# Kernel optimization log

Measured on AMD Instinct MI355X. Metric: run time of the kernel, lower is better.

The kernel has to match this reference:

```python
import jax, jax.numpy as jnp
import numpy as np
import math

D_MODEL = 2048
D_STATE = 16
EXPAND = 2
D_INNER = D_MODEL * EXPAND          # 4096
DT_RANK = math.ceil(D_MODEL / 16)   # 128
BATCH, SEQ_LEN = 2, 512


def setup_inputs() -> dict:
    key = jax.random.key(0)
    ks = jax.random.split(key, 6)
    x = jax.random.normal(ks[0], (BATCH, SEQ_LEN, D_INNER), dtype=jnp.float32)
    # A_log such that A = -exp(A_log) is a stable negative-real decay
    A_log = jnp.log(jax.random.uniform(ks[1], (D_INNER, D_STATE), minval=0.5, maxval=16.0, dtype=jnp.float32))
    D = jnp.ones((D_INNER,), dtype=jnp.float32)
    x_proj_w = 0.02 * jax.random.normal(ks[2], (DT_RANK + 2 * D_STATE, D_INNER), dtype=jnp.float32)
    dt_init_std = DT_RANK ** -0.5
    dt_proj_w = jax.random.uniform(ks[3], (D_INNER, DT_RANK), minval=-dt_init_std, maxval=dt_init_std, dtype=jnp.float32)
    # inverse-softplus init of dt bias, dt ~ loguniform[1e-3, 0.1]
    dt = jnp.exp(jax.random.uniform(ks[4], (D_INNER,), dtype=jnp.float32) * (math.log(0.1) - math.log(0.001)) + math.log(0.001))
    dt = jnp.clip(dt, 1e-4, None)
    dt_proj_b = dt + jnp.log(-jnp.expm1(-dt))
    return {"x": x, "A_log": A_log, "D": D, "x_proj_w": x_proj_w,
            "dt_proj_w": dt_proj_w, "dt_proj_b": dt_proj_b}


def reference(x, A_log, D, x_proj_w, dt_proj_w, dt_proj_b):
    # x: (b, l, d)
    A = -jnp.exp(A_log)                                  # (d, n)
    xp = jnp.einsum('bld,rd->blr', x, x_proj_w)          # (b, l, dt_rank + 2n)
    dt_in = xp[..., :DT_RANK]
    B = xp[..., DT_RANK:DT_RANK + D_STATE]               # (b, l, n)
    C = xp[..., DT_RANK + D_STATE:]                      # (b, l, n)
    dt = jax.nn.softplus(jnp.einsum('blr,dr->bld', dt_in, dt_proj_w) + dt_proj_b)  # (b, l, d)
    dA = jnp.exp(dt[..., None] * A)                      # (b, l, d, n)
    dBx = dt[..., None] * B[:, :, None, :] * x[..., None]  # (b, l, d, n)

    def step(h, inp):
        dA_t, dBx_t, C_t = inp                           # (b,d,n), (b,d,n), (b,n)
        h = dA_t * h + dBx_t
        y = jnp.einsum('bdn,bn->bd', h, C_t)
        return h, y

    h0 = jnp.zeros((x.shape[0], D_INNER, D_STATE), dtype=x.dtype)
    _, ys = jax.lax.scan(step, h0,
                         (jnp.moveaxis(dA, 1, 0), jnp.moveaxis(dBx, 1, 0), jnp.moveaxis(C, 1, 0)))
    y = jnp.moveaxis(ys, 0, 1) + D * x                   # (b, l, d)
    return y
```

## Files before the change

### kernel.cpp

```cpp
#include <hip/hip_runtime.h>
#include <math.h>

#define BATCH   2
#define SEQLEN  512
#define DI      4096
#define DS      16
#define RDT     128
#define RTOT    160
#define BL      1024

#define KSPLIT  16

typedef __bf16 bf16;
typedef bf16  bf16x8 __attribute__((ext_vector_type(8)));
typedef bf16  bf16x4 __attribute__((ext_vector_type(4)));
typedef float f32x4  __attribute__((ext_vector_type(4)));

__global__ __launch_bounds__(256) void cast_bf16(const float* __restrict__ src,
                                                 bf16* __restrict__ dst, int n4) {
  const int i = blockIdx.x * 256 + threadIdx.x;
  if (i < n4) {
    float4 v = ((const float4*)src)[i];
    bf16x4 o;
    o[0] = (bf16)v.x; o[1] = (bf16)v.y; o[2] = (bf16)v.z; o[3] = (bf16)v.w;
    *(bf16x4*)(dst + 4 * (size_t)i) = o;
  }
}

__global__ __launch_bounds__(256) void gemm_xp_mfma(const float* __restrict__ x,
                                                    const bf16* __restrict__ Wb,
                                                    float* __restrict__ part) {
  const int tid = threadIdx.x;
  const int w = tid >> 6;
  const int lane = tid & 63;
  const int m = lane & 15;
  const int q = lane >> 4;
  const int row0 = blockIdx.x * 64 + 16 * w;
  const int k0 = blockIdx.y * (DI / KSPLIT);

  f32x4 acc[10] = {};

  const float* ap = x + (size_t)(row0 + m) * DI + k0 + 8 * q;
  const bf16*  bp = Wb + (size_t)m * DI + k0 + 8 * q;

#pragma unroll 2
  for (int kk = 0; kk < DI / KSPLIT; kk += 32) {
    float4 a0 = *(const float4*)(ap + kk);
    float4 a1 = *(const float4*)(ap + kk + 4);
    bf16x8 af;
    af[0] = (bf16)a0.x; af[1] = (bf16)a0.y; af[2] = (bf16)a0.z; af[3] = (bf16)a0.w;
    af[4] = (bf16)a1.x; af[5] = (bf16)a1.y; af[6] = (bf16)a1.z; af[7] = (bf16)a1.w;
#pragma unroll
    for (int nt = 0; nt < 10; ++nt) {
      bf16x8 bf = *(const bf16x8*)(bp + (size_t)nt * 16 * DI + kk);
      acc[nt] = __builtin_amdgcn_mfma_f32_16x16x32_bf16(af, bf, acc[nt], 0, 0, 0);
    }
  }

  float* p = part + (size_t)blockIdx.y * (BL * RTOT);
#pragma unroll
  for (int nt = 0; nt < 10; ++nt)
#pragma unroll
    for (int r = 0; r < 4; ++r)
      p[(size_t)(row0 + 4 * q + r) * RTOT + nt * 16 + m] = acc[nt][r];
}

__global__ __launch_bounds__(256) void reduce_xp(const float* __restrict__ part,
                                                 float* __restrict__ xp,
                                                 bf16* __restrict__ dtinb) {
  const int o = blockIdx.x * 256 + threadIdx.x;
  float s = 0.f;
#pragma unroll
  for (int k = 0; k < KSPLIT; ++k) s += part[(size_t)k * (BL * RTOT) + o];
  xp[o] = s;
  const int row = o / RTOT;
  const int col = o - row * RTOT;
  if (col < RDT) dtinb[row * RDT + col] = (bf16)s;
}

__global__ __launch_bounds__(256) void gemm_dt_mfma(const bf16* __restrict__ Ab,
                                                    const bf16* __restrict__ Bb,
                                                    const float* __restrict__ dtb,
                                                    float* __restrict__ dtbuf) {
  const int tid = threadIdx.x;
  const int w = tid >> 6;
  const int lane = tid & 63;
  const int m = lane & 15;
  const int q = lane >> 4;
  const int row0 = blockIdx.x * 64 + 16 * w;
  const int n0 = blockIdx.y * 128;

  f32x4 acc[8] = {};

  const bf16* apb = Ab + (size_t)(row0 + m) * RDT + 8 * q;
  const bf16* bpb = Bb + (size_t)(n0 + m) * RDT + 8 * q;

#pragma unroll
  for (int kk = 0; kk < RDT; kk += 32) {
    bf16x8 af = *(const bf16x8*)(apb + kk);
#pragma unroll
    for (int nt = 0; nt < 8; ++nt) {
      bf16x8 bf = *(const bf16x8*)(bpb + (size_t)nt * 16 * RDT + kk);
      acc[nt] = __builtin_amdgcn_mfma_f32_16x16x32_bf16(af, bf, acc[nt], 0, 0, 0);
    }
  }

#pragma unroll
  for (int nt = 0; nt < 8; ++nt) {
    const int col = n0 + nt * 16 + m;
    const float bias = dtb[col];
#pragma unroll
    for (int r = 0; r < 4; ++r) {
      const float z = acc[nt][r] + bias;
      const float sp = (z > 20.f) ? z : __logf(1.f + __expf(z));
      dtbuf[(size_t)(row0 + 4 * q + r) * DI + col] = sp;
    }
  }
}

__device__ __forceinline__ float row16_reduce_add(float p) {
  p += __int_as_float(__builtin_amdgcn_update_dpp(
      0, __float_as_int(p), 0x111, 0xf, 0xf, true));
  p += __int_as_float(__builtin_amdgcn_update_dpp(
      0, __float_as_int(p), 0x112, 0xf, 0xf, true));
  p += __int_as_float(__builtin_amdgcn_update_dpp(
      0, __float_as_int(p), 0x114, 0xf, 0xf, true));
  p += __int_as_float(__builtin_amdgcn_update_dpp(
      0, __float_as_int(p), 0x118, 0xf, 0xf, true));
  return p;
}

#define TC  64
#define TCP 66
#define NCH (SEQLEN / TC)

__global__ __launch_bounds__(256) void scan_kernel(const float* __restrict__ x,
                                                   const float* __restrict__ A_log,
                                                   const float* __restrict__ Dvec,
                                                   const float* __restrict__ xp,
                                                   const float* __restrict__ dtbuf,
                                                   float* __restrict__ out) {
  __shared__ __align__(16) float2 dxS[16][TCP];
  __shared__ __align__(16) float2 bcS[16][TCP];
  __shared__ __align__(16) float  yS[TC][16];

  const int bid = blockIdx.x;
  const int b = bid >> 8;
  const int d0 = (bid & 255) * 16;
  const int tid = threadIdx.x;
  const int n = tid & 15;
  const int dc = tid >> 4;
  const int d = d0 + dc;

  const float A = -expf(A_log[d * DS + n]);
  const float Dd = Dvec[d];

  const int lt = tid >> 2;
  const int lf = (tid & 3) * 4;
  const int rowbase = b * SEQLEN;

  float4 rdt, rx, rB, rC;
  {
    const int row = rowbase + lt;
    rdt = *(const float4*)&dtbuf[row * DI + d0 + lf];
    rx  = *(const float4*)&x[row * DI + d0 + lf];
    rB  = *(const float4*)&xp[row * RTOT + RDT + lf];
    rC  = *(const float4*)&xp[row * RTOT + RDT + DS + lf];
  }

  float h = 0.f;

  for (int c = 0; c < NCH; ++c) {
    if (c > 0) __syncthreads();

    {
      const float rdta[4] = {rdt.x, rdt.y, rdt.z, rdt.w};
      const float rxa[4]  = {rx.x, rx.y, rx.z, rx.w};
      const float rBa[4]  = {rB.x, rB.y, rB.z, rB.w};
      const float rCa[4]  = {rC.x, rC.y, rC.z, rC.w};
#pragma unroll
      for (int j = 0; j < 4; ++j) {
        dxS[lf + j][lt] = make_float2(rdta[j], rxa[j]);
        bcS[lf + j][lt] = make_float2(rBa[j], rCa[j]);
      }
    }

    if (c > 0) {
      const int prow = rowbase + (c - 1) * TC + lt;
      float4 yv = *(const float4*)&yS[lt][lf];
      *(float4*)&out[prow * DI + d0 + lf] = yv;
    }

    __syncthreads();

    if (c < NCH - 1) {
      const int row = rowbase + (c + 1) * TC + lt;
      rdt = *(const float4*)&dtbuf[row * DI + d0 + lf];
      rx  = *(const float4*)&x[row * DI + d0 + lf];
      rB  = *(const float4*)&xp[row * RTOT + RDT + lf];
      rC  = *(const float4*)&xp[row * RTOT + RDT + DS + lf];
    }

#pragma unroll 8
    for (int t = 0; t < TC; t += 2) {
      const float4 dx2 = *(const float4*)&dxS[dc][t];
      const float4 bc2 = *(const float4*)&bcS[n][t];
      const float dA0 = __expf(dx2.x * A);
      h = fmaf(dA0, h, dx2.x * dx2.y * bc2.x);
      const float p0 = row16_reduce_add(h * bc2.y);
      if (n == 15) yS[t][dc] = fmaf(Dd, dx2.y, p0);
      const float dA1 = __expf(dx2.z * A);
      h = fmaf(dA1, h, dx2.z * dx2.w * bc2.z);
      const float p1 = row16_reduce_add(h * bc2.w);
      if (n == 15) yS[t + 1][dc] = fmaf(Dd, dx2.w, p1);
    }
  }

  __syncthreads();
  {
    const int prow = rowbase + (NCH - 1) * TC + lt;
    float4 yv = *(const float4*)&yS[lt][lf];
    *(float4*)&out[prow * DI + d0 + lf] = yv;
  }
}

extern "C" void kernel_launch(void* const* d_in, const int* in_sizes, int n_in,
                              void* d_out, int out_size, void* d_ws, size_t ws_size,
                              hipStream_t stream) {
  const float* x     = (const float*)d_in[0];
  const float* A_log = (const float*)d_in[1];
  const float* Dv    = (const float*)d_in[2];
  const float* W     = (const float*)d_in[3];
  const float* dtw   = (const float*)d_in[4];
  const float* dtb   = (const float*)d_in[5];
  float* out = (float*)d_out;

  char* ws = (char*)d_ws;
  float* dtbuf = (float*)ws;
  float* part  = (float*)ws;
  float* xp    = (float*)(ws + 16777216);
  bf16*  Wb    = (bf16*)(ws + 16777216 + 655360);
  bf16*  dtwb  = (bf16*)(ws + 16777216 + 655360 + 1310720);
  bf16*  dtinb = (bf16*)(ws + 16777216 + 655360 + 1310720 + 1048576);

  cast_bf16<<<dim3(640), 256, 0, stream>>>(W, Wb, RTOT * DI / 4);
  cast_bf16<<<dim3(512), 256, 0, stream>>>(dtw, dtwb, DI * RDT / 4);
  gemm_xp_mfma<<<dim3(16, KSPLIT), 256, 0, stream>>>(x, Wb, part);
  reduce_xp<<<dim3(640), 256, 0, stream>>>(part, xp, dtinb);
  gemm_dt_mfma<<<dim3(16, 32), 256, 0, stream>>>(dtinb, dtwb, dtb, dtbuf);
  scan_kernel<<<dim3(512), 256, 0, stream>>>(x, A_log, Dv, xp, dtbuf, out);
}
```

Baseline: 165.7 us.

## Fuse dt projection GEMM and softplus into the scan kernel

Removes the separate dt GEMM kernel and its 16MB fp32 dt buffer. Each scan block now computes its own 64x16 dt tile per chunk with MFMA from bf16 dt_in and dt_proj weights held in registers, then applies softplus. Also merges the two cast kernels, doubles the K-split for the xp GEMM, vectorizes the reduction into a compact B/C buffer, and restructures the scan loop into batches of 8 with the DPP reductions deferred. This trades a global write and read of dt for some extra MFMA and softplus work inside the latency-bound scan, plus a larger partial-sum reduction.

```diff
diff --git a/kernel.cpp b/kernel.cpp
--- a/kernel.cpp
+++ b/kernel.cpp
@@ -9,22 +9,28 @@
 #define RTOT    160
 #define BL      1024
 
-#define KSPLIT  16
+#define KSPLIT  32
+#define KSL     (DI / KSPLIT)
 
 typedef __bf16 bf16;
 typedef bf16  bf16x8 __attribute__((ext_vector_type(8)));
 typedef bf16  bf16x4 __attribute__((ext_vector_type(4)));
 typedef float f32x4  __attribute__((ext_vector_type(4)));
 
-__global__ __launch_bounds__(256) void cast_bf16(const float* __restrict__ src,
-                                                 bf16* __restrict__ dst, int n4) {
+__global__ __launch_bounds__(256) void cast_both(const float* __restrict__ W,
+                                                 const float* __restrict__ dtw,
+                                                 bf16* __restrict__ Wb,
+                                                 bf16* __restrict__ dtwb) {
   const int i = blockIdx.x * 256 + threadIdx.x;
-  if (i < n4) {
-    float4 v = ((const float4*)src)[i];
-    bf16x4 o;
-    o[0] = (bf16)v.x; o[1] = (bf16)v.y; o[2] = (bf16)v.z; o[3] = (bf16)v.w;
-    *(bf16x4*)(dst + 4 * (size_t)i) = o;
-  }
+  const float4* src;
+  bf16* dst;
+  int j;
+  if (i < RTOT * DI / 4) { src = (const float4*)W;   dst = Wb;   j = i; }
+  else                   { src = (const float4*)dtw; dst = dtwb; j = i - RTOT * DI / 4; }
+  float4 v = src[j];
+  bf16x4 o;
+  o[0] = (bf16)v.x; o[1] = (bf16)v.y; o[2] = (bf16)v.z; o[3] = (bf16)v.w;
+  *(bf16x4*)(dst + 4 * (size_t)j) = o;
 }
 
 __global__ __launch_bounds__(256) void gemm_xp_mfma(const float* __restrict__ x,
@@ -36,15 +42,15 @@
   const int m = lane & 15;
   const int q = lane >> 4;
   const int row0 = blockIdx.x * 64 + 16 * w;
-  const int k0 = blockIdx.y * (DI / KSPLIT);
+  const int k0 = blockIdx.y * KSL;
 
   f32x4 acc[10] = {};
 
   const float* ap = x + (size_t)(row0 + m) * DI + k0 + 8 * q;
   const bf16*  bp = Wb + (size_t)m * DI + k0 + 8 * q;
 
-#pragma unroll 2
-  for (int kk = 0; kk < DI / KSPLIT; kk += 32) {
+#pragma unroll
+  for (int kk = 0; kk < KSL; kk += 32) {
     float4 a0 = *(const float4*)(ap + kk);
     float4 a1 = *(const float4*)(ap + kk + 4);
     bf16x8 af;
@@ -52,8 +58,8 @@
     af[4] = (bf16)a1.x; af[5] = (bf16)a1.y; af[6] = (bf16)a1.z; af[7] = (bf16)a1.w;
 #pragma unroll
     for (int nt = 0; nt < 10; ++nt) {
-      bf16x8 bf = *(const bf16x8*)(bp + (size_t)nt * 16 * DI + kk);
-      acc[nt] = __builtin_amdgcn_mfma_f32_16x16x32_bf16(af, bf, acc[nt], 0, 0, 0);
+      bf16x8 bfv = *(const bf16x8*)(bp + (size_t)nt * 16 * DI + kk);
+      acc[nt] = __builtin_amdgcn_mfma_f32_16x16x32_bf16(af, bfv, acc[nt], 0, 0, 0);
     }
   }
 
@@ -66,55 +72,23 @@
 }
 
 __global__ __launch_bounds__(256) void reduce_xp(const float* __restrict__ part,
-                                                 float* __restrict__ xp,
+                                                 float* __restrict__ BCf,
                                                  bf16* __restrict__ dtinb) {
-  const int o = blockIdx.x * 256 + threadIdx.x;
-  float s = 0.f;
-#pragma unroll
-  for (int k = 0; k < KSPLIT; ++k) s += part[(size_t)k * (BL * RTOT) + o];
-  xp[o] = s;
+  const int o = (blockIdx.x * 256 + threadIdx.x) * 4;
+  float4 s = make_float4(0.f, 0.f, 0.f, 0.f);
+#pragma unroll
+  for (int k = 0; k < KSPLIT; ++k) {
+    float4 v = *(const float4*)&part[(size_t)k * (BL * RTOT) + o];
+    s.x += v.x; s.y += v.y; s.z += v.z; s.w += v.w;
+  }
   const int row = o / RTOT;
   const int col = o - row * RTOT;
-  if (col < RDT) dtinb[row * RDT + col] = (bf16)s;
-}
-
-__global__ __launch_bounds__(256) void gemm_dt_mfma(const bf16* __restrict__ Ab,
-                                                    const bf16* __restrict__ Bb,
-                                                    const float* __restrict__ dtb,
-                                                    float* __restrict__ dtbuf) {
-  const int tid = threadIdx.x;
-  const int w = tid >> 6;
-  const int lane = tid & 63;
-  const int m = lane & 15;
-  const int q = lane >> 4;
-  const int row0 = blockIdx.x * 64 + 16 * w;
-  const int n0 = blockIdx.y * 128;
-
-  f32x4 acc[8] = {};
-
-  const bf16* apb = Ab + (size_t)(row0 + m) * RDT + 8 * q;
-  const bf16* bpb = Bb + (size_t)(n0 + m) * RDT + 8 * q;
-
-#pragma unroll
-  for (int kk = 0; kk < RDT; kk += 32) {
-    bf16x8 af = *(const bf16x8*)(apb + kk);
-#pragma unroll
-    for (int nt = 0; nt < 8; ++nt) {
-      bf16x8 bf = *(const bf16x8*)(bpb + (size_t)nt * 16 * RDT + kk);
-      acc[nt] = __builtin_amdgcn_mfma_f32_16x16x32_bf16(af, bf, acc[nt], 0, 0, 0);
-    }
-  }
-
-#pragma unroll
-  for (int nt = 0; nt < 8; ++nt) {
-    const int col = n0 + nt * 16 + m;
-    const float bias = dtb[col];
-#pragma unroll
-    for (int r = 0; r < 4; ++r) {
-      const float z = acc[nt][r] + bias;
-      const float sp = (z > 20.f) ? z : __logf(1.f + __expf(z));
-      dtbuf[(size_t)(row0 + 4 * q + r) * DI + col] = sp;
-    }
+  if (col < RDT) {
+    bf16x4 ob;
+    ob[0] = (bf16)s.x; ob[1] = (bf16)s.y; ob[2] = (bf16)s.z; ob[3] = (bf16)s.w;
+    *(bf16x4*)(dtinb + (size_t)row * RDT + col) = ob;
+  } else {
+    *(float4*)&BCf[(size_t)row * 32 + (col - RDT)] = s;
   }
 }
 
@@ -131,18 +105,22 @@
 }
 
 #define TC  64
-#define TCP 66
+#define TCP 68
 #define NCH (SEQLEN / TC)
 
-__global__ __launch_bounds__(256) void scan_kernel(const float* __restrict__ x,
-                                                   const float* __restrict__ A_log,
-                                                   const float* __restrict__ Dvec,
-                                                   const float* __restrict__ xp,
-                                                   const float* __restrict__ dtbuf,
-                                                   float* __restrict__ out) {
-  __shared__ __align__(16) float2 dxS[16][TCP];
-  __shared__ __align__(16) float2 bcS[16][TCP];
-  __shared__ __align__(16) float  yS[TC][16];
+__global__ __launch_bounds__(256) void scan_fused(const float* __restrict__ x,
+                                                  const float* __restrict__ A_log,
+                                                  const float* __restrict__ Dvec,
+                                                  const float* __restrict__ BCf,
+                                                  const bf16* __restrict__ dtin,
+                                                  const bf16* __restrict__ dtwb,
+                                                  const float* __restrict__ dtb,
+                                                  float* __restrict__ out) {
+  __shared__ __align__(16) float dtS[16][TCP];
+  __shared__ __align__(16) float xS[16][TCP];
+  __shared__ __align__(16) float BS[16][TCP];
+  __shared__ __align__(16) float CS[16][TCP];
+  __shared__ __align__(16) float yS[TC][16];
 
   const int bid = blockIdx.x;
   const int b = bid >> 8;
@@ -151,21 +129,34 @@
   const int n = tid & 15;
   const int dc = tid >> 4;
   const int d = d0 + dc;
+  const int w = tid >> 6;
+  const int m = tid & 15;
+  const int q = (tid >> 4) & 3;
 
   const float A = -expf(A_log[d * DS + n]);
   const float Dd = Dvec[d];
+  const float bias = dtb[d0 + m];
+
+  bf16x8 bfragW[4];
+#pragma unroll
+  for (int k = 0; k < 4; ++k)
+    bfragW[k] = *(const bf16x8*)(dtwb + (size_t)(d0 + m) * RDT + 32 * k + 8 * q);
 
   const int lt = tid >> 2;
   const int lf = (tid & 3) * 4;
   const int rowbase = b * SEQLEN;
 
-  float4 rdt, rx, rB, rC;
+  bf16x8 afrag[4];
+  float4 rx, rB, rC;
   {
+    const int arow = rowbase + 16 * w + m;
+#pragma unroll
+    for (int k = 0; k < 4; ++k)
+      afrag[k] = *(const bf16x8*)(dtin + (size_t)arow * RDT + 32 * k + 8 * q);
     const int row = rowbase + lt;
-    rdt = *(const float4*)&dtbuf[row * DI + d0 + lf];
-    rx  = *(const float4*)&x[row * DI + d0 + lf];
-    rB  = *(const float4*)&xp[row * RTOT + RDT + lf];
-    rC  = *(const float4*)&xp[row * RTOT + RDT + DS + lf];
+    rx = *(const float4*)&x[(size_t)row * DI + d0 + lf];
+    rB = *(const float4*)&BCf[row * 32 + lf];
+    rC = *(const float4*)&BCf[row * 32 + 16 + lf];
   }
 
   float h = 0.f;
@@ -174,45 +165,80 @@
     if (c > 0) __syncthreads();
 
     {
-      const float rdta[4] = {rdt.x, rdt.y, rdt.z, rdt.w};
-      const float rxa[4]  = {rx.x, rx.y, rx.z, rx.w};
-      const float rBa[4]  = {rB.x, rB.y, rB.z, rB.w};
-      const float rCa[4]  = {rC.x, rC.y, rC.z, rC.w};
+      f32x4 acc = {};
+#pragma unroll
+      for (int k = 0; k < 4; ++k)
+        acc = __builtin_amdgcn_mfma_f32_16x16x32_bf16(afrag[k], bfragW[k], acc, 0, 0, 0);
+#pragma unroll
+      for (int r = 0; r < 4; ++r) {
+        const float z = acc[r] + bias;
+        dtS[m][16 * w + 4 * q + r] = (z > 20.f) ? z : __logf(1.f + __expf(z));
+      }
+    }
+    {
+      const float rxa[4] = {rx.x, rx.y, rx.z, rx.w};
+      const float rBa[4] = {rB.x, rB.y, rB.z, rB.w};
+      const float rCa[4] = {rC.x, rC.y, rC.z, rC.w};
 #pragma unroll
       for (int j = 0; j < 4; ++j) {
-        dxS[lf + j][lt] = make_float2(rdta[j], rxa[j]);
-        bcS[lf + j][lt] = make_float2(rBa[j], rCa[j]);
-      }
-    }
-
+        xS[lf + j][lt] = rxa[j];
+        BS[lf + j][lt] = rBa[j];
+        CS[lf + j][lt] = rCa[j];
+      }
+    }
     if (c > 0) {
       const int prow = rowbase + (c - 1) * TC + lt;
       float4 yv = *(const float4*)&yS[lt][lf];
-      *(float4*)&out[prow * DI + d0 + lf] = yv;
+      *(float4*)&out[(size_t)prow * DI + d0 + lf] = yv;
     }
 
     __syncthreads();
 
     if (c < NCH - 1) {
+      const int arow = rowbase + (c + 1) * TC + 16 * w + m;
+#pragma unroll
+      for (int k = 0; k < 4; ++k)
+        afrag[k] = *(const bf16x8*)(dtin + (size_t)arow * RDT + 32 * k + 8 * q);
       const int row = rowbase + (c + 1) * TC + lt;
-      rdt = *(const float4*)&dtbuf[row * DI + d0 + lf];
-      rx  = *(const float4*)&x[row * DI + d0 + lf];
-      rB  = *(const float4*)&xp[row * RTOT + RDT + lf];
-      rC  = *(const float4*)&xp[row * RTOT + RDT + DS + lf];
-    }
-
-#pragma unroll 8
-    for (int t = 0; t < TC; t += 2) {
-      const float4 dx2 = *(const float4*)&dxS[dc][t];
-      const float4 bc2 = *(const float4*)&bcS[n][t];
-      const float dA0 = __expf(dx2.x * A);
-      h = fmaf(dA0, h, dx2.x * dx2.y * bc2.x);
-      const float p0 = row16_reduce_add(h * bc2.y);
-      if (n == 15) yS[t][dc] = fmaf(Dd, dx2.y, p0);
-      const float dA1 = __expf(dx2.z * A);
-      h = fmaf(dA1, h, dx2.z * dx2.w * bc2.z);
-      const float p1 = row16_reduce_add(h * bc2.w);
-      if (n == 15) yS[t + 1][dc] = fmaf(Dd, dx2.w, p1);
+      rx = *(const float4*)&x[(size_t)row * DI + d0 + lf];
+      rB = *(const float4*)&BCf[row * 32 + lf];
+      rC = *(const float4*)&BCf[row * 32 + 16 + lf];
+    }
+
+    for (int g = 0; g < 8; ++g) {
+      const int t0 = 8 * g;
+      const float4 dv0 = *(const float4*)&dtS[dc][t0];
+      const float4 dv1 = *(const float4*)&dtS[dc][t0 + 4];
+      const float4 xv0 = *(const float4*)&xS[dc][t0];
+      const float4 xv1 = *(const float4*)&xS[dc][t0 + 4];
+      const float4 Bv0 = *(const float4*)&BS[n][t0];
+      const float4 Bv1 = *(const float4*)&BS[n][t0 + 4];
+      const float4 Cv0 = *(const float4*)&CS[n][t0];
+      const float4 Cv1 = *(const float4*)&CS[n][t0 + 4];
+      const float dt[8] = {dv0.x, dv0.y, dv0.z, dv0.w, dv1.x, dv1.y, dv1.z, dv1.w};
+      const float xv[8] = {xv0.x, xv0.y, xv0.z, xv0.w, xv1.x, xv1.y, xv1.z, xv1.w};
+      const float Bv[8] = {Bv0.x, Bv0.y, Bv0.z, Bv0.w, Bv1.x, Bv1.y, Bv1.z, Bv1.w};
+      const float Cv[8] = {Cv0.x, Cv0.y, Cv0.z, Cv0.w, Cv1.x, Cv1.y, Cv1.z, Cv1.w};
+
+      float e[8], u[8], p[8];
+#pragma unroll
+      for (int j = 0; j < 8; ++j) {
+        e[j] = __expf(dt[j] * A);
+        u[j] = dt[j] * xv[j] * Bv[j];
+      }
+#pragma unroll
+      for (int j = 0; j < 8; ++j) {
+        h = fmaf(e[j], h, u[j]);
+        p[j] = h * Cv[j];
+      }
+#pragma unroll
+      for (int j = 0; j < 8; ++j)
+        p[j] = row16_reduce_add(p[j]);
+      if (n == 15) {
+#pragma unroll
+        for (int j = 0; j < 8; ++j)
+          yS[t0 + j][dc] = fmaf(Dd, xv[j], p[j]);
+      }
     }
   }
 
@@ -220,7 +246,7 @@
   {
     const int prow = rowbase + (NCH - 1) * TC + lt;
     float4 yv = *(const float4*)&yS[lt][lf];
-    *(float4*)&out[prow * DI + d0 + lf] = yv;
+    *(float4*)&out[(size_t)prow * DI + d0 + lf] = yv;
   }
 }
 
@@ -236,17 +262,14 @@
   float* out = (float*)d_out;
 
   char* ws = (char*)d_ws;
-  float* dtbuf = (float*)ws;
   float* part  = (float*)ws;
-  float* xp    = (float*)(ws + 16777216);
-  bf16*  Wb    = (bf16*)(ws + 16777216 + 655360);
-  bf16*  dtwb  = (bf16*)(ws + 16777216 + 655360 + 1310720);
-  bf16*  dtinb = (bf16*)(ws + 16777216 + 655360 + 1310720 + 1048576);
-
-  cast_bf16<<<dim3(640), 256, 0, stream>>>(W, Wb, RTOT * DI / 4);
-  cast_bf16<<<dim3(512), 256, 0, stream>>>(dtw, dtwb, DI * RDT / 4);
+  bf16*  Wb    = (bf16*)(ws + 20971520);
+  bf16*  dtwb  = (bf16*)(ws + 22282240);
+  float* BCf   = (float*)(ws + 23330816);
+  bf16*  dtinb = (bf16*)(ws + 23461888);
+
+  cast_both<<<dim3(1152), 256, 0, stream>>>(W, dtw, Wb, dtwb);
   gemm_xp_mfma<<<dim3(16, KSPLIT), 256, 0, stream>>>(x, Wb, part);
-  reduce_xp<<<dim3(640), 256, 0, stream>>>(part, xp, dtinb);
-  gemm_dt_mfma<<<dim3(16, 32), 256, 0, stream>>>(dtinb, dtwb, dtb, dtbuf);
-  scan_kernel<<<dim3(512), 256, 0, stream>>>(x, A_log, Dv, xp, dtbuf, out);
-}
+  reduce_xp<<<dim3(160), 256, 0, stream>>>(part, BCf, dtinb);
+  scan_fused<<<dim3(512), 256, 0, stream>>>(x, A_log, Dv, BCf, dtinb, dtwb, dtb, out);
+}
```

Result: faster. 136.0 us (-17.9%).
